# Kernel optimization log

Hardware: AMD Instinct MI355X
Metric: run time of the kernel (lower is better)

Reference implementation:

```python
import jax, jax.numpy as jnp
import numpy as np

B, H, W, C = 2, 64, 128, 256
HEADS, K, HIDDEN = 8, 9, 1024
HD = C // HEADS
EPS = 1e-5


def _ln(z, g, b):
    m = z.mean(-1, keepdims=True)
    v = ((z - m) ** 2).mean(-1, keepdims=True)
    return (z - m) / jnp.sqrt(v + EPS) * g + b


def _bilinear(img, coords):
    # img: [hd, H, W]; coords: [H, W, K, 2] in [-1, 1] (x=width, y=height), align_corners=True
    Hh, Ww = img.shape[1], img.shape[2]
    cx = (coords[..., 0] + 1.0) * 0.5 * (Ww - 1)
    cy = (coords[..., 1] + 1.0) * 0.5 * (Hh - 1)
    x0 = jnp.floor(cx); y0 = jnp.floor(cy)
    wx = cx - x0; wy = cy - y0
    x0i = jnp.clip(x0, 0, Ww - 1).astype(jnp.int32)
    x1i = jnp.clip(x0 + 1, 0, Ww - 1).astype(jnp.int32)
    y0i = jnp.clip(y0, 0, Hh - 1).astype(jnp.int32)
    y1i = jnp.clip(y0 + 1, 0, Hh - 1).astype(jnp.int32)
    g = lambda yi, xi: img[:, yi, xi]  # [hd, H, W, K]
    return (g(y0i, x0i) * (1 - wy) * (1 - wx) + g(y0i, x1i) * (1 - wy) * wx
            + g(y1i, x0i) * wy * (1 - wx) + g(y1i, x1i) * wy * wx)


def setup_inputs() -> dict:
    key = jax.random.key(0)
    ks = jax.random.split(key, 12)
    s = 0.02
    return {
        "x": jax.random.normal(ks[0], (B, H * W, C), jnp.float32),
        "ref_point": jax.random.uniform(ks[1], (1, H, W, K, 2), jnp.float32, -1.0, 1.0),
        "ln1_g": jnp.ones((C,), jnp.float32), "ln1_b": jnp.zeros((C,), jnp.float32),
        "w_v": jax.random.normal(ks[2], (C, C), jnp.float32) * s, "b_v": jnp.zeros((C,), jnp.float32),
        "w_off": jax.random.normal(ks[3], (C, HEADS * K * 2), jnp.float32) * s, "b_off": jnp.zeros((HEADS * K * 2,), jnp.float32),
        "w_attn": jax.random.normal(ks[4], (C, HEADS * K), jnp.float32) * s, "b_attn": jnp.zeros((HEADS * K,), jnp.float32),
        "w_out": jax.random.normal(ks[5], (C, C), jnp.float32) * s, "b_out": jnp.zeros((C,), jnp.float32),
        "ln2_g": jnp.ones((C,), jnp.float32), "ln2_b": jnp.zeros((C,), jnp.float32),
        "w1": jax.random.normal(ks[6], (C, HIDDEN), jnp.float32) * s, "b1": jnp.zeros((HIDDEN,), jnp.float32),
        "w_dw": jax.random.normal(ks[7], (HIDDEN, 1, 3, 3), jnp.float32) * s, "b_dw": jnp.zeros((HIDDEN,), jnp.float32),
        "w2": jax.random.normal(ks[8], (HIDDEN, C), jnp.float32) * s, "b2": jnp.zeros((C,), jnp.float32),
    }


def reference(x, ref_point, ln1_g, ln1_b, w_v, b_v, w_off, b_off, w_attn, b_attn,
              w_out, b_out, ln2_g, ln2_b, w1, b1, w_dw, b_dw, w2, b2):
    # --- Sphere deformable self-attention branch ---
    xn = _ln(x, ln1_g, ln1_b).reshape(B, H, W, C)
    v = (xn @ w_v + b_v).reshape(B, H, W, HEADS, HD)
    v = jnp.transpose(v, (0, 3, 4, 1, 2))                               # [B, heads, hd, H, W]
    off = (xn @ w_off + b_off).reshape(B, H, W, HEADS, K, 2)
    locs = ref_point[:, :, :, None, :, :] + off                          # [B, H, W, heads, K, 2]
    locs = jnp.transpose(locs, (0, 3, 1, 2, 4, 5))                       # [B, heads, H, W, K, 2]
    attn = jax.nn.softmax((xn @ w_attn + b_attn).reshape(B, H, W, HEADS, K), axis=-1)
    sampled = jax.vmap(jax.vmap(_bilinear))(v, locs)                     # [B, heads, hd, H, W, K]
    agg = jnp.einsum('bndhwk,bhwnk->bhwnd', sampled, attn).reshape(B, H, W, C)
    x = x + ((agg @ w_out) + b_out).reshape(B, H * W, C)
    # --- LeFF branch: linear -> GELU -> circular-pad depthwise conv -> GELU -> linear ---
    y = _ln(x, ln2_g, ln2_b)
    h = jax.nn.gelu(y @ w1 + b1, approximate=False).reshape(B, H, W, HIDDEN)
    h = jnp.transpose(h, (0, 3, 1, 2))                                   # NCHW
    h = jnp.pad(h, ((0, 0), (0, 0), (0, 0), (1, 1)), mode='wrap')        # circular pad along width
    h = jnp.pad(h, ((0, 0), (0, 0), (1, 1), (0, 0)))                     # zero pad along height
    h = jax.lax.conv_general_dilated(h, w_dw, (1, 1), 'VALID',
                                     feature_group_count=HIDDEN,
                                     dimension_numbers=('NCHW', 'OIHW', 'NCHW'))
    h = jax.nn.gelu(h + b_dw[None, :, None, None], approximate=False)
    h = jnp.transpose(h, (0, 2, 3, 1)).reshape(B, H * W, HIDDEN)
    return x + h @ w2 + b2
```

## Files before the change

### kernel.cpp

```cpp
#include <hip/hip_runtime.h>
#include <hip/hip_bf16.h>
#include <type_traits>

constexpr int Bc = 2, Hc = 64, Wc = 128, Cc = 256;
constexpr int HEADS = 8, KPT = 9, HIDDEN = 1024;
constexpr int HD = Cc / HEADS;
constexpr int NPIX = Hc * Wc;
constexpr int Mrows = Bc * NPIX;
constexpr int NQKV = 512;

typedef __attribute__((ext_vector_type(4))) float f32x4;
typedef __attribute__((ext_vector_type(8))) short bf16x8;

__device__ __forceinline__ float bf2f(unsigned short u) {
    union { unsigned int i; float f; } c; c.i = ((unsigned int)u) << 16; return c.f;
}
__device__ __forceinline__ unsigned short f2bf(float f) {
    __hip_bfloat16 h = __float2bfloat16(f);
    return *reinterpret_cast<unsigned short*>(&h);
}
__device__ __forceinline__ float gelu_exact(float x) {
    return 0.5f * x * (1.0f + erff(x * 0.70710678118654752f));
}
__device__ __forceinline__ void gl2lds16(const void* g, void* l) {
    __builtin_amdgcn_global_load_lds(
        (const __attribute__((address_space(1))) unsigned int*)g,
        (__attribute__((address_space(3))) unsigned int*)l, 16, 0, 0);
}

template<typename TO>
__global__ __launch_bounds__(256) void ln_kernel(const float* __restrict__ in,
        const float* __restrict__ g, const float* __restrict__ b,
        TO* __restrict__ out) {
    const int r = blockIdx.x * 4 + (threadIdx.x >> 6);
    const int l = threadIdx.x & 63;
    const size_t base = (size_t)r * Cc + l * 4;
    const float4 v = *reinterpret_cast<const float4*>(in + base);
    float s  = v.x + v.y + v.z + v.w;
    float s2 = v.x * v.x + v.y * v.y + v.z * v.z + v.w * v.w;
    #pragma unroll
    for (int o = 32; o > 0; o >>= 1) { s += __shfl_down(s, o); s2 += __shfl_down(s2, o); }
    s = __shfl(s, 0); s2 = __shfl(s2, 0);
    const float mean = s * (1.0f / Cc);
    const float var  = s2 * (1.0f / Cc) - mean * mean;
    const float rstd = rsqrtf(var + 1e-5f);
    const float4 gv = *reinterpret_cast<const float4*>(g + l * 4);
    const float4 bv = *reinterpret_cast<const float4*>(b + l * 4);
    const float o0 = (v.x - mean) * rstd * gv.x + bv.x;
    const float o1 = (v.y - mean) * rstd * gv.y + bv.y;
    const float o2 = (v.z - mean) * rstd * gv.z + bv.z;
    const float o3 = (v.w - mean) * rstd * gv.w + bv.w;
    if constexpr (std::is_same<TO, float>::value) {
        *reinterpret_cast<float4*>(out + base) = make_float4(o0, o1, o2, o3);
    } else {
        ushort4 o;
        o.x = f2bf(o0); o.y = f2bf(o1); o.z = f2bf(o2); o.w = f2bf(o3);
        *reinterpret_cast<ushort4*>(out + base) = o;
    }
}

__global__ __launch_bounds__(256) void prep_weights(
        const float* __restrict__ w_v, const float* __restrict__ b_v,
        const float* __restrict__ w_off, const float* __restrict__ b_off,
        const float* __restrict__ w_attn, const float* __restrict__ b_attn,
        const float* __restrict__ w_out, const float* __restrict__ w1,
        const float* __restrict__ w2, const float* __restrict__ w_dw,
        unsigned short* __restrict__ qkvT, float* __restrict__ qkvB,
        unsigned short* __restrict__ woutT, unsigned short* __restrict__ w1T,
        unsigned short* __restrict__ w2T, float* __restrict__ wdwT) {
    const int blk = blockIdx.x;
    const int t = threadIdx.x;
    if (blk < NQKV) {
        const int n = blk;
        float val = 0.0f;
        if (n < 256)       val = w_v[t * 256 + n];
        else if (n < 400)  val = w_off[t * 144 + (n - 256)];
        else if (n < 472)  val = w_attn[t * 72 + (n - 400)];
        qkvT[n * 256 + t] = f2bf(val);
        if (t == 0) {
            float bv = 0.0f;
            if (n < 256)      bv = b_v[n];
            else if (n < 400) bv = b_off[n - 256];
            else if (n < 472) bv = b_attn[n - 400];
            qkvB[n] = bv;
        }
    } else if (blk < NQKV + 256) {
        const int n = blk - NQKV;
        woutT[n * 256 + t] = f2bf(w_out[t * 256 + n]);
    } else if (blk < NQKV + 256 + 1024) {
        const int n = blk - (NQKV + 256);
        w1T[n * 256 + t] = f2bf(w1[t * 1024 + n]);
    } else if (blk < NQKV + 256 + 1024 + 256) {
        const int n = blk - (NQKV + 256 + 1024);
        #pragma unroll
        for (int k = t; k < 1024; k += 256)
            w2T[n * 1024 + k] = f2bf(w2[k * 256 + n]);
    } else {
        const int j = blk - (NQKV + 256 + 1024 + 256);
        #pragma unroll
        for (int c = t; c < HIDDEN; c += 256)
            wdwT[j * HIDDEN + c] = w_dw[c * 9 + j];
    }
}

template<int BN, bool GELU, bool RESID, typename TO>
__global__ __launch_bounds__(512) void mfma_gemm(
        const unsigned short* __restrict__ A,
        const unsigned short* __restrict__ BT,
        const float* __restrict__ bias,
        const float* __restrict__ resid,
        TO* __restrict__ Out,
        int N, int K) {
    constexpr int WCOLS = (BN == 128) ? 4 : 2;
    constexpr int WROWS = 8 / WCOLS;
    constexpr int MI = 128 / (WROWS * 16);
    constexpr int NI = BN / (WCOLS * 16);
    constexpr int ACH = 2;
    constexpr int BCH = (BN / 8) / 8;
    constexpr int LA = ACH + BCH;
    constexpr int BUFB = 16384 + BN * 128;
    __shared__ __align__(16) char lds[2 * BUFB];
    const int t = threadIdx.x;
    const int w = t >> 6;
    const int l = t & 63;
    const int row0 = blockIdx.x * 128;
    const int col0 = blockIdx.y * BN;
    const int wr = (w / WCOLS) * (MI * 16);
    const int wc = (w % WCOLS) * (NI * 16);

    const int srow = l >> 3;
    const int selem = ((l & 7) ^ srow) * 8;

    auto stage = [&](char* buf, int k0) {
        unsigned short* As_ = (unsigned short*)buf;
        unsigned short* Bs_ = (unsigned short*)(buf + 16384);
        #pragma unroll
        for (int i = 0; i < ACH; ++i) {
            const int c = w + i * 8;
            const int row = c * 8 + srow;
            gl2lds16(A + (size_t)(row0 + row) * K + k0 + selem, As_ + c * 512);
        }
        #pragma unroll
        for (int i = 0; i < BCH; ++i) {
            const int c = w + i * 8;
            const int row = c * 8 + srow;
            gl2lds16(BT + (size_t)(col0 + row) * K + k0 + selem, Bs_ + c * 512);
        }
    };

    f32x4 acc[MI][NI] = {};
    const int nt = K / 64;

    stage(lds, 0);
    stage(lds + BUFB, 64);

    for (int tt = 0; tt < nt; ++tt) {
        if (tt + 1 < nt) {
            if constexpr (LA == 4) asm volatile("s_waitcnt vmcnt(4)" ::: "memory");
            else                   asm volatile("s_waitcnt vmcnt(3)" ::: "memory");
        } else {
            asm volatile("s_waitcnt vmcnt(0)" ::: "memory");
        }
        __builtin_amdgcn_s_barrier();
        __builtin_amdgcn_sched_barrier(0);

        const char* Ab = lds + (size_t)(tt & 1) * BUFB;
        const char* Bb = Ab + 16384;
        #pragma unroll
        for (int ks = 0; ks < 2; ++ks) {
            const int kb = ks * 64 + (l >> 4) * 16;
            bf16x8 af[MI], bfr[NI];
            #pragma unroll
            for (int mi = 0; mi < MI; ++mi) {
                const int row = wr + mi * 16 + (l & 15);
                af[mi] = *(const bf16x8*)(Ab + row * 128 + (kb ^ ((row & 7) << 4)));
            }
            #pragma unroll
            for (int ni = 0; ni < NI; ++ni) {
                const int row = wc + ni * 16 + (l & 15);
                bfr[ni] = *(const bf16x8*)(Bb + row * 128 + (kb ^ ((row & 7) << 4)));
            }
            #pragma unroll
            for (int mi = 0; mi < MI; ++mi)
                #pragma unroll
                for (int ni = 0; ni < NI; ++ni)
                    acc[mi][ni] = __builtin_amdgcn_mfma_f32_16x16x32_bf16(
                        af[mi], bfr[ni], acc[mi][ni], 0, 0, 0);
        }
        __builtin_amdgcn_s_barrier();
        __builtin_amdgcn_sched_barrier(0);
        if (tt + 2 < nt) stage(lds + (size_t)(tt & 1) * BUFB, (tt + 2) * 64);
    }

    const int lrow = (l >> 4) * 4;
    const int lcol = l & 15;
    #pragma unroll
    for (int ni = 0; ni < NI; ++ni) {
        const int col = wc + ni * 16 + lcol;
        const float bb = bias[col0 + col];
        #pragma unroll
        for (int mi = 0; mi < MI; ++mi) {
            #pragma unroll
            for (int r = 0; r < 4; ++r) {
                const int row = wr + mi * 16 + lrow + r;
                float v = acc[mi][ni][r] + bb;
                if constexpr (GELU) v = gelu_exact(v);
                if constexpr (std::is_same<TO, unsigned short>::value) {
                    *(unsigned short*)(lds + row * 256 + ((col * 2) ^ ((row & 7) << 4))) = f2bf(v);
                } else {
                    *(float*)(lds + row * 256 + ((col * 4) ^ ((row & 7) << 4))) = v;
                }
            }
        }
    }
    __syncthreads();
    const int ck = t & 15;
    #pragma unroll
    for (int it = 0; it < 4; ++it) {
        const int row = (t >> 4) + it * 32;
        const int bo = ck * 16;
        if constexpr (std::is_same<TO, unsigned short>::value) {
            const int4 val = *(const int4*)(lds + row * 256 + (bo ^ ((row & 7) << 4)));
            *(int4*)(Out + (size_t)(row0 + row) * N + col0 + bo / 2) = val;
        } else {
            float4 val = *(const float4*)(lds + row * 256 + (bo ^ ((row & 7) << 4)));
            if constexpr (RESID) {
                const float4 rv = *(const float4*)(resid + (size_t)(row0 + row) * N + col0 + bo / 4);
                val.x += rv.x; val.y += rv.y; val.z += rv.z; val.w += rv.w;
            }
            *(float4*)((float*)Out + (size_t)(row0 + row) * N + col0 + bo / 4) = val;
        }
    }
}

__global__ __launch_bounds__(256) void sample_kernel(const unsigned short* __restrict__ F,
        const float* __restrict__ refp, unsigned short* __restrict__ agg) {
    constexpr int PPB = 4;
    constexpr int nblk = Mrows / PPB;
    const int bid = blockIdx.x;
    const int qi = (bid & 7) * (nblk / 8) + (bid >> 3);
    const int m0 = qi * PPB;
    const int b = m0 / NPIX;
    const int pix0 = m0 - b * NPIX;
    const int t = threadIdx.x;
    __shared__ int4   s_idx[PPB][72];
    __shared__ float4 s_w[PPB][72];
    __shared__ float  s_lg[PPB][72];

    for (int idx = t; idx < PPB * 72; idx += 256) {
        const int p = idx / 72, hk = idx - p * 72;
        const int head = hk / 9, k = hk - head * 9;
        const int m = m0 + p, pix = pix0 + p;
        const size_t fb = (size_t)m * NQKV;
        const unsigned int ou = *(const unsigned int*)(F + fb + 256 + head * 18 + k * 2);
        const float ox = __uint_as_float(ou << 16);
        const float oy = __uint_as_float(ou & 0xffff0000u);
        const float2 rr = *(const float2*)(refp + ((size_t)pix * KPT + k) * 2);
        const float cx = (rr.x + ox + 1.0f) * 0.5f * (Wc - 1);
        const float cy = (rr.y + oy + 1.0f) * 0.5f * (Hc - 1);
        const float fx = floorf(cx), fy = floorf(cy);
        const float wx = cx - fx, wy = cy - fy;
        const int x0 = min(max((int)fx, 0), Wc - 1);
        const int x1 = min(max((int)fx + 1, 0), Wc - 1);
        const int y0 = min(max((int)fy, 0), Hc - 1);
        const int y1 = min(max((int)fy + 1, 0), Hc - 1);
        s_idx[p][hk] = make_int4(y0 * Wc + x0, y0 * Wc + x1, y1 * Wc + x0, y1 * Wc + x1);
        s_w[p][hk] = make_float4((1.0f - wy) * (1.0f - wx), (1.0f - wy) * wx,
                                 wy * (1.0f - wx), wy * wx);
        s_lg[p][hk] = bf2f(F[fb + 400 + hk]);
    }
    __syncthreads();
    for (int idx = t; idx < PPB * 72; idx += 256) {
        const int p = idx / 72, hk = idx - p * 72;
        const int h9 = (hk / 9) * 9;
        float mx = -1e30f;
        #pragma unroll
        for (int k = 0; k < 9; ++k) mx = fmaxf(mx, s_lg[p][h9 + k]);
        float sm = 0.0f;
        #pragma unroll
        for (int k = 0; k < 9; ++k) sm += __expf(s_lg[p][h9 + k] - mx);
        const float a = __expf(s_lg[p][hk] - mx) / sm;
        float4 w = s_w[p][hk];
        w.x *= a; w.y *= a; w.z *= a; w.w *= a;
        s_w[p][hk] = w;
    }
    __syncthreads();
    const int p = t >> 6, tl = t & 63;
    const int head = tl >> 3, dq = tl & 7;
    const unsigned short* vb = F + (size_t)b * NPIX * NQKV + head * HD + dq * 4;
    float a0 = 0.f, a1 = 0.f, a2 = 0.f, a3 = 0.f;
    #pragma unroll
    for (int k = 0; k < 9; ++k) {
        const int hk = head * 9 + k;
        const int4   ix = s_idx[p][hk];
        const float4 ww = s_w[p][hk];
        {
            const uint2 u = *(const uint2*)(vb + (size_t)ix.x * NQKV);
            a0 += __uint_as_float(u.x << 16) * ww.x;
            a1 += __uint_as_float(u.x & 0xffff0000u) * ww.x;
            a2 += __uint_as_float(u.y << 16) * ww.x;
            a3 += __uint_as_float(u.y & 0xffff0000u) * ww.x;
        }
        {
            const uint2 u = *(const uint2*)(vb + (size_t)ix.y * NQKV);
            a0 += __uint_as_float(u.x << 16) * ww.y;
            a1 += __uint_as_float(u.x & 0xffff0000u) * ww.y;
            a2 += __uint_as_float(u.y << 16) * ww.y;
            a3 += __uint_as_float(u.y & 0xffff0000u) * ww.y;
        }
        {
            const uint2 u = *(const uint2*)(vb + (size_t)ix.z * NQKV);
            a0 += __uint_as_float(u.x << 16) * ww.z;
            a1 += __uint_as_float(u.x & 0xffff0000u) * ww.z;
            a2 += __uint_as_float(u.y << 16) * ww.z;
            a3 += __uint_as_float(u.y & 0xffff0000u) * ww.z;
        }
        {
            const uint2 u = *(const uint2*)(vb + (size_t)ix.w * NQKV);
            a0 += __uint_as_float(u.x << 16) * ww.w;
            a1 += __uint_as_float(u.x & 0xffff0000u) * ww.w;
            a2 += __uint_as_float(u.y << 16) * ww.w;
            a3 += __uint_as_float(u.y & 0xffff0000u) * ww.w;
        }
    }
    ushort4 o;
    o.x = f2bf(a0); o.y = f2bf(a1); o.z = f2bf(a2); o.w = f2bf(a3);
    *reinterpret_cast<ushort4*>(agg + (size_t)(m0 + p) * Cc + tl * 4) = o;
}

__global__ __launch_bounds__(256) void dwconv_kernel(const unsigned short* __restrict__ h,
        const float* __restrict__ wdwT, const float* __restrict__ bdw,
        unsigned short* __restrict__ h2) {
    constexpr int NQ = 4;
    constexpr int nblk = Mrows / NQ;
    const int bid = blockIdx.x;
    const int qi = (bid & 7) * (nblk / 8) + (bid >> 3);
    const int m0 = qi * NQ;
    const int b = m0 / NPIX;
    const int pix0 = m0 - b * NPIX;
    const int y = pix0 / Wc, x0 = pix0 - y * Wc;
    const int t = threadIdx.x;
    const int c0 = t * 4;

    float wreg[9][4];
    #pragma unroll
    for (int j = 0; j < 9; ++j) {
        const float4 wv = *reinterpret_cast<const float4*>(wdwT + j * HIDDEN + c0);
        wreg[j][0] = wv.x; wreg[j][1] = wv.y; wreg[j][2] = wv.z; wreg[j][3] = wv.w;
    }

    float acc[NQ][4] = {};
    #pragma unroll
    for (int dy = -1; dy <= 1; ++dy) {
        const int yy = y + dy;
        if (yy < 0 || yy >= Hc) continue;
        const size_t rowbase = ((size_t)b * NPIX + (size_t)yy * Wc) * HIDDEN + c0;
        #pragma unroll
        for (int j = 0; j < NQ + 2; ++j) {
            const int xx = (x0 + j - 1 + Wc) & (Wc - 1);
            const ushort4 hv = *reinterpret_cast<const ushort4*>(h + rowbase + (size_t)xx * HIDDEN);
            const float f0 = bf2f(hv.x), f1 = bf2f(hv.y), f2 = bf2f(hv.z), f3 = bf2f(hv.w);
            #pragma unroll
            for (int q = 0; q < NQ; ++q) {
                if (q >= j - 2 && q <= j) {
                    const int wj = (dy + 1) * 3 + (j - q);
                    acc[q][0] += f0 * wreg[wj][0];
                    acc[q][1] += f1 * wreg[wj][1];
                    acc[q][2] += f2 * wreg[wj][2];
                    acc[q][3] += f3 * wreg[wj][3];
                }
            }
        }
    }
    const float4 bb = *reinterpret_cast<const float4*>(bdw + c0);
    #pragma unroll
    for (int q = 0; q < NQ; ++q) {
        ushort4 o;
        o.x = f2bf(gelu_exact(acc[q][0] + bb.x));
        o.y = f2bf(gelu_exact(acc[q][1] + bb.y));
        o.z = f2bf(gelu_exact(acc[q][2] + bb.z));
        o.w = f2bf(gelu_exact(acc[q][3] + bb.w));
        *reinterpret_cast<ushort4*>(h2 + (size_t)(m0 + q) * HIDDEN + c0) = o;
    }
}

extern "C" void kernel_launch(void* const* d_in, const int* in_sizes, int n_in,
                              void* d_out, int out_size, void* d_ws, size_t ws_size,
                              hipStream_t stream) {
    const float* x      = (const float*)d_in[0];
    const float* refp   = (const float*)d_in[1];
    const float* ln1_g  = (const float*)d_in[2];
    const float* ln1_b  = (const float*)d_in[3];
    const float* w_v    = (const float*)d_in[4];
    const float* b_v    = (const float*)d_in[5];
    const float* w_off  = (const float*)d_in[6];
    const float* b_off  = (const float*)d_in[7];
    const float* w_attn = (const float*)d_in[8];
    const float* b_attn = (const float*)d_in[9];
    const float* w_out  = (const float*)d_in[10];
    const float* b_out  = (const float*)d_in[11];
    const float* ln2_g  = (const float*)d_in[12];
    const float* ln2_b  = (const float*)d_in[13];
    const float* w1     = (const float*)d_in[14];
    const float* b1     = (const float*)d_in[15];
    const float* w_dw   = (const float*)d_in[16];
    const float* b_dw   = (const float*)d_in[17];
    const float* w2     = (const float*)d_in[18];
    const float* b2     = (const float*)d_in[19];
    float* out = (float*)d_out;

    char* wsb = (char*)d_ws;
    unsigned short* xnR = (unsigned short*)(wsb);
    unsigned short* F   = (unsigned short*)(wsb + (8ull  << 20));
    unsigned short* h   = (unsigned short*)(wsb + (8ull  << 20));
    unsigned short* h2  = (unsigned short*)(wsb + (40ull << 20));
    size_t woff = 72ull << 20;
    unsigned short* qkvT = (unsigned short*)(wsb + woff); woff += (size_t)NQKV * 256 * 2;
    unsigned short* woutT= (unsigned short*)(wsb + woff); woff += 256 * 256 * 2;
    unsigned short* w1T  = (unsigned short*)(wsb + woff); woff += 1024 * 256 * 2;
    unsigned short* w2T  = (unsigned short*)(wsb + woff); woff += 256 * 1024 * 2;
    float*          wdwT = (float*)(wsb + woff);          woff += 9 * 1024 * 4;
    float*          qkvB = (float*)(wsb + woff);

    prep_weights<<<NQKV + 256 + 1024 + 256 + 9, 256, 0, stream>>>(
        w_v, b_v, w_off, b_off, w_attn, b_attn, w_out, w1, w2, w_dw,
        qkvT, qkvB, woutT, w1T, w2T, wdwT);
    ln_kernel<unsigned short><<<Mrows / 4, 256, 0, stream>>>(x, ln1_g, ln1_b, xnR);
    mfma_gemm<128, false, false, unsigned short><<<dim3(Mrows / 128, NQKV / 128), 512, 0, stream>>>(
        xnR, qkvT, qkvB, nullptr, F, NQKV, 256);
    sample_kernel<<<Mrows / 4, 256, 0, stream>>>(F, refp, xnR);
    mfma_gemm<64, false, true, float><<<dim3(Mrows / 128, 256 / 64), 512, 0, stream>>>(
        xnR, woutT, b_out, x, out, 256, 256);
    ln_kernel<unsigned short><<<Mrows / 4, 256, 0, stream>>>(out, ln2_g, ln2_b, xnR);
    mfma_gemm<128, true, false, unsigned short><<<dim3(Mrows / 128, 1024 / 128), 512, 0, stream>>>(
        xnR, w1T, b1, nullptr, h, 1024, 256);
    dwconv_kernel<<<Mrows / 4, 256, 0, stream>>>(h, wdwT, b_dw, h2);
    mfma_gemm<64, false, true, float><<<dim3(Mrows / 128, 256 / 64), 512, 0, stream>>>(
        h2, w2T, b2, out, out, 256, 1024);
}
```

Measured before the change: 132.4 us.

## Fuse LN1 into weight prep and fuse w_out GEMM with residual and LN2

Folds the first LayerNorm into the weight-prep launch as extra blocks, which removes one kernel launch. It also adds a dedicated kernel in which each block owns 64 full rows across all 256 output columns. That kernel computes the w_out GEMM, adds bias and the residual, writes the fp32 output and applies LN2 in its epilogue, so the separate LN2 pass no longer has to re-read `out`. The trade-off is that the fused GEMM launches only 256 blocks with a larger LDS footprint, and the workspace buffers are re-laid out so several of them alias.

```diff
diff --git a/kernel.cpp b/kernel.cpp
--- a/kernel.cpp
+++ b/kernel.cpp
@@ -28,38 +28,9 @@
         (__attribute__((address_space(3))) unsigned int*)l, 16, 0, 0);
 }
 
-template<typename TO>
-__global__ __launch_bounds__(256) void ln_kernel(const float* __restrict__ in,
-        const float* __restrict__ g, const float* __restrict__ b,
-        TO* __restrict__ out) {
-    const int r = blockIdx.x * 4 + (threadIdx.x >> 6);
-    const int l = threadIdx.x & 63;
-    const size_t base = (size_t)r * Cc + l * 4;
-    const float4 v = *reinterpret_cast<const float4*>(in + base);
-    float s  = v.x + v.y + v.z + v.w;
-    float s2 = v.x * v.x + v.y * v.y + v.z * v.z + v.w * v.w;
-    #pragma unroll
-    for (int o = 32; o > 0; o >>= 1) { s += __shfl_down(s, o); s2 += __shfl_down(s2, o); }
-    s = __shfl(s, 0); s2 = __shfl(s2, 0);
-    const float mean = s * (1.0f / Cc);
-    const float var  = s2 * (1.0f / Cc) - mean * mean;
-    const float rstd = rsqrtf(var + 1e-5f);
-    const float4 gv = *reinterpret_cast<const float4*>(g + l * 4);
-    const float4 bv = *reinterpret_cast<const float4*>(b + l * 4);
-    const float o0 = (v.x - mean) * rstd * gv.x + bv.x;
-    const float o1 = (v.y - mean) * rstd * gv.y + bv.y;
-    const float o2 = (v.z - mean) * rstd * gv.z + bv.z;
-    const float o3 = (v.w - mean) * rstd * gv.w + bv.w;
-    if constexpr (std::is_same<TO, float>::value) {
-        *reinterpret_cast<float4*>(out + base) = make_float4(o0, o1, o2, o3);
-    } else {
-        ushort4 o;
-        o.x = f2bf(o0); o.y = f2bf(o1); o.z = f2bf(o2); o.w = f2bf(o3);
-        *reinterpret_cast<ushort4*>(out + base) = o;
-    }
-}
-
-__global__ __launch_bounds__(256) void prep_weights(
+__global__ __launch_bounds__(256) void prepln_kernel(
+        const float* __restrict__ x, const float* __restrict__ ln1_g,
+        const float* __restrict__ ln1_b, unsigned short* __restrict__ xn,
         const float* __restrict__ w_v, const float* __restrict__ b_v,
         const float* __restrict__ w_off, const float* __restrict__ b_off,
         const float* __restrict__ w_attn, const float* __restrict__ b_attn,
@@ -68,8 +39,30 @@
         unsigned short* __restrict__ qkvT, float* __restrict__ qkvB,
         unsigned short* __restrict__ woutT, unsigned short* __restrict__ w1T,
         unsigned short* __restrict__ w2T, float* __restrict__ wdwT) {
-    const int blk = blockIdx.x;
     const int t = threadIdx.x;
+    if (blockIdx.x < Mrows / 4) {
+        const int r = blockIdx.x * 4 + (t >> 6);
+        const int l = t & 63;
+        const size_t base = (size_t)r * Cc + l * 4;
+        const float4 v = *reinterpret_cast<const float4*>(x + base);
+        float s  = v.x + v.y + v.z + v.w;
+        float s2 = v.x * v.x + v.y * v.y + v.z * v.z + v.w * v.w;
+        #pragma unroll
+        for (int o = 32; o > 0; o >>= 1) { s += __shfl_down(s, o); s2 += __shfl_down(s2, o); }
+        s = __shfl(s, 0); s2 = __shfl(s2, 0);
+        const float mean = s * (1.0f / Cc);
+        const float rstd = rsqrtf(s2 * (1.0f / Cc) - mean * mean + 1e-5f);
+        const float4 gv = *reinterpret_cast<const float4*>(ln1_g + l * 4);
+        const float4 bv = *reinterpret_cast<const float4*>(ln1_b + l * 4);
+        ushort4 o;
+        o.x = f2bf((v.x - mean) * rstd * gv.x + bv.x);
+        o.y = f2bf((v.y - mean) * rstd * gv.y + bv.y);
+        o.z = f2bf((v.z - mean) * rstd * gv.z + bv.z);
+        o.w = f2bf((v.w - mean) * rstd * gv.w + bv.w);
+        *reinterpret_cast<ushort4*>(xn + base) = o;
+        return;
+    }
+    const int blk = blockIdx.x - Mrows / 4;
     if (blk < NQKV) {
         const int n = blk;
         float val = 0.0f;
@@ -233,6 +226,122 @@
     }
 }
 
+__global__ __launch_bounds__(512) void wout_ln2_kernel(
+        const unsigned short* __restrict__ A,
+        const unsigned short* __restrict__ BT,
+        const float* __restrict__ bias,
+        const float* __restrict__ resid,
+        const float* __restrict__ g2, const float* __restrict__ b2,
+        float* __restrict__ Out,
+        unsigned short* __restrict__ Y) {
+    constexpr int BM = 64, K = 256;
+    constexpr int ABYTES = BM * 128;
+    constexpr int BUFB = ABYTES + 256 * 128;
+    __shared__ __align__(16) char lds[2 * BUFB];
+    const int t = threadIdx.x;
+    const int w = t >> 6;
+    const int l = t & 63;
+    const int row0 = blockIdx.x * BM;
+    const int wr = (w >> 2) * 32;
+    const int wc = (w & 3) * 64;
+
+    const int srow = l >> 3;
+    const int selem = ((l & 7) ^ srow) * 8;
+
+    auto stage = [&](char* buf, int k0) {
+        unsigned short* As_ = (unsigned short*)buf;
+        unsigned short* Bs_ = (unsigned short*)(buf + ABYTES);
+        {
+            const int row = w * 8 + srow;
+            gl2lds16(A + (size_t)(row0 + row) * K + k0 + selem, As_ + w * 512);
+        }
+        #pragma unroll
+        for (int i = 0; i < 4; ++i) {
+            const int c = w + i * 8;
+            const int row = c * 8 + srow;
+            gl2lds16(BT + (size_t)row * K + k0 + selem, Bs_ + c * 512);
+        }
+    };
+
+    f32x4 acc[2][4] = {};
+    stage(lds, 0);
+    stage(lds + BUFB, 64);
+
+    for (int tt = 0; tt < 4; ++tt) {
+        if (tt + 1 < 4) asm volatile("s_waitcnt vmcnt(5)" ::: "memory");
+        else            asm volatile("s_waitcnt vmcnt(0)" ::: "memory");
+        __builtin_amdgcn_s_barrier();
+        __builtin_amdgcn_sched_barrier(0);
+
+        const char* Ab = lds + (size_t)(tt & 1) * BUFB;
+        const char* Bb = Ab + ABYTES;
+        #pragma unroll
+        for (int ks = 0; ks < 2; ++ks) {
+            const int kb = ks * 64 + (l >> 4) * 16;
+            bf16x8 af[2], bfr[4];
+            #pragma unroll
+            for (int mi = 0; mi < 2; ++mi) {
+                const int row = wr + mi * 16 + (l & 15);
+                af[mi] = *(const bf16x8*)(Ab + row * 128 + (kb ^ ((row & 7) << 4)));
+            }
+            #pragma unroll
+            for (int ni = 0; ni < 4; ++ni) {
+                const int row = wc + ni * 16 + (l & 15);
+                bfr[ni] = *(const bf16x8*)(Bb + row * 128 + (kb ^ ((row & 7) << 4)));
+            }
+            #pragma unroll
+            for (int mi = 0; mi < 2; ++mi)
+                #pragma unroll
+                for (int ni = 0; ni < 4; ++ni)
+                    acc[mi][ni] = __builtin_amdgcn_mfma_f32_16x16x32_bf16(
+                        af[mi], bfr[ni], acc[mi][ni], 0, 0, 0);
+        }
+        __builtin_amdgcn_s_barrier();
+        __builtin_amdgcn_sched_barrier(0);
+        if (tt + 2 < 4) stage(lds + (size_t)(tt & 1) * BUFB, (tt + 2) * 64);
+    }
+
+    const int lrow = (l >> 4) * 4;
+    const int lcol = l & 15;
+    #pragma unroll
+    for (int ni = 0; ni < 4; ++ni) {
+        const int col = wc + ni * 16 + lcol;
+        const float bb = bias[col];
+        #pragma unroll
+        for (int mi = 0; mi < 2; ++mi) {
+            #pragma unroll
+            for (int r = 0; r < 4; ++r) {
+                const int row = wr + mi * 16 + lrow + r;
+                *(float*)(lds + row * 1024 + ((col * 4) ^ ((row & 7) << 4))) = acc[mi][ni][r] + bb;
+            }
+        }
+    }
+    __syncthreads();
+    const float4 gv = *reinterpret_cast<const float4*>(g2 + l * 4);
+    const float4 bv = *reinterpret_cast<const float4*>(b2 + l * 4);
+    #pragma unroll
+    for (int it = 0; it < 8; ++it) {
+        const int r = w + it * 8;
+        float4 v = *(const float4*)(lds + r * 1024 + ((l * 16) ^ ((r & 7) << 4)));
+        const float4 rv = *(const float4*)(resid + (size_t)(row0 + r) * Cc + l * 4);
+        v.x += rv.x; v.y += rv.y; v.z += rv.z; v.w += rv.w;
+        float s  = v.x + v.y + v.z + v.w;
+        float s2 = v.x * v.x + v.y * v.y + v.z * v.z + v.w * v.w;
+        #pragma unroll
+        for (int o = 32; o > 0; o >>= 1) { s += __shfl_down(s, o); s2 += __shfl_down(s2, o); }
+        s = __shfl(s, 0); s2 = __shfl(s2, 0);
+        const float mean = s * (1.0f / Cc);
+        const float rstd = rsqrtf(s2 * (1.0f / Cc) - mean * mean + 1e-5f);
+        *(float4*)(Out + (size_t)(row0 + r) * Cc + l * 4) = v;
+        ushort4 o;
+        o.x = f2bf((v.x - mean) * rstd * gv.x + bv.x);
+        o.y = f2bf((v.y - mean) * rstd * gv.y + bv.y);
+        o.z = f2bf((v.z - mean) * rstd * gv.z + bv.z);
+        o.w = f2bf((v.w - mean) * rstd * gv.w + bv.w);
+        *(ushort4*)(Y + (size_t)(row0 + r) * Cc + l * 4) = o;
+    }
+}
+
 __global__ __launch_bounds__(256) void sample_kernel(const unsigned short* __restrict__ F,
         const float* __restrict__ refp, unsigned short* __restrict__ agg) {
     constexpr int PPB = 4;
@@ -410,11 +519,12 @@
     float* out = (float*)d_out;
 
     char* wsb = (char*)d_ws;
-    unsigned short* xnR = (unsigned short*)(wsb);
-    unsigned short* F   = (unsigned short*)(wsb + (8ull  << 20));
-    unsigned short* h   = (unsigned short*)(wsb + (8ull  << 20));
-    unsigned short* h2  = (unsigned short*)(wsb + (40ull << 20));
-    size_t woff = 72ull << 20;
+    unsigned short* Abuf = (unsigned short*)(wsb);
+    unsigned short* F    = (unsigned short*)(wsb + (8ull  << 20));
+    unsigned short* ybuf = (unsigned short*)(wsb + (8ull  << 20));
+    unsigned short* h    = (unsigned short*)(wsb + (32ull << 20));
+    unsigned short* h2   = (unsigned short*)(wsb);
+    size_t woff = 64ull << 20;
     unsigned short* qkvT = (unsigned short*)(wsb + woff); woff += (size_t)NQKV * 256 * 2;
     unsigned short* woutT= (unsigned short*)(wsb + woff); woff += 256 * 256 * 2;
     unsigned short* w1T  = (unsigned short*)(wsb + woff); woff += 1024 * 256 * 2;
@@ -422,18 +532,17 @@
     float*          wdwT = (float*)(wsb + woff);          woff += 9 * 1024 * 4;
     float*          qkvB = (float*)(wsb + woff);
 
-    prep_weights<<<NQKV + 256 + 1024 + 256 + 9, 256, 0, stream>>>(
+    prepln_kernel<<<Mrows / 4 + NQKV + 256 + 1024 + 256 + 9, 256, 0, stream>>>(
+        x, ln1_g, ln1_b, Abuf,
         w_v, b_v, w_off, b_off, w_attn, b_attn, w_out, w1, w2, w_dw,
         qkvT, qkvB, woutT, w1T, w2T, wdwT);
-    ln_kernel<unsigned short><<<Mrows / 4, 256, 0, stream>>>(x, ln1_g, ln1_b, xnR);
     mfma_gemm<128, false, false, unsigned short><<<dim3(Mrows / 128, NQKV / 128), 512, 0, stream>>>(
-        xnR, qkvT, qkvB, nullptr, F, NQKV, 256);
-    sample_kernel<<<Mrows / 4, 256, 0, stream>>>(F, refp, xnR);
-    mfma_gemm<64, false, true, float><<<dim3(Mrows / 128, 256 / 64), 512, 0, stream>>>(
-        xnR, woutT, b_out, x, out, 256, 256);
-    ln_kernel<unsigned short><<<Mrows / 4, 256, 0, stream>>>(out, ln2_g, ln2_b, xnR);
+        Abuf, qkvT, qkvB, nullptr, F, NQKV, 256);
+    sample_kernel<<<Mrows / 4, 256, 0, stream>>>(F, refp, Abuf);
+    wout_ln2_kernel<<<Mrows / 64, 512, 0, stream>>>(
+        Abuf, woutT, b_out, x, ln2_g, ln2_b, out, ybuf);
     mfma_gemm<128, true, false, unsigned short><<<dim3(Mrows / 128, 1024 / 128), 512, 0, stream>>>(
-        xnR, w1T, b1, nullptr, h, 1024, 256);
+        ybuf, w1T, b1, nullptr, h, 1024, 256);
     dwconv_kernel<<<Mrows / 4, 256, 0, stream>>>(h, wdwT, b_dw, h2);
     mfma_gemm<64, false, true, float><<<dim3(Mrows / 128, 256 / 64), 512, 0, stream>>>(
         h2, w2T, b2, out, out, 256, 1024);
```

Result: faster. 127.7 us (-3.5%).
